# Performance work log

Hardware: AMD Instinct MI355X
Metric: run time of the kernel (lower is better)

Reference implementation:

```python
import jax, jax.numpy as jnp
import numpy as np

N_NODES = 65536
N_PER = 1024      # nodes per graph
NUM_GRAPHS = 64
N_EDGES = 1048576
IN_DIM = 192
PE_DIM = 64
HIDDEN = 256
LATENT = 128
POOL_RATIO = 0.5
K_PER = int(np.ceil(POOL_RATIO * N_PER))  # 512 kept per graph


def setup_inputs() -> dict:
    key = jax.random.key(0)
    ks = jax.random.split(key, 12)
    x_raw = jax.random.normal(ks[0], (N_NODES, IN_DIM), dtype=jnp.float32)
    sincos_pe = jax.random.normal(ks[1], (N_NODES, PE_DIM), dtype=jnp.float32)
    edge_index = jax.random.randint(ks[2], (2, N_EDGES), 0, N_NODES, dtype=jnp.int64)
    batch = (jnp.arange(N_NODES, dtype=jnp.int64) // N_PER)
    eps = jax.random.normal(ks[3], (N_NODES, LATENT), dtype=jnp.float32)
    # learned parameters (GCNConv: Linear no-bias weight + separate bias; TopKPooling weight)
    def glorot(k, shape):
        lim = float(np.sqrt(6.0 / (shape[0] + shape[1])))
        return jax.random.uniform(k, shape, jnp.float32, -lim, lim)
    W1 = glorot(ks[4], (IN_DIM + PE_DIM, HIDDEN))
    b1 = jnp.zeros((HIDDEN,), jnp.float32)
    Wmu = glorot(ks[5], (HIDDEN, LATENT))
    bmu = jnp.zeros((LATENT,), jnp.float32)
    Wlv = glorot(ks[6], (HIDDEN, LATENT))
    blv = jnp.zeros((LATENT,), jnp.float32)
    w_pool = jax.random.uniform(ks[7], (LATENT,), jnp.float32, -1.0, 1.0) / np.sqrt(LATENT)
    return {"x_raw": x_raw, "sincos_pe": sincos_pe, "edge_index": edge_index,
            "batch": batch, "eps": eps, "W1": W1, "b1": b1, "Wmu": Wmu,
            "bmu": bmu, "Wlv": Wlv, "blv": blv, "w_pool": w_pool}


def _gcn_conv(x, W, b, src, dst, n):
    # PyG GCNConv: x' = D^{-1/2}(A+I)D^{-1/2} (x W) + b, self-loops already in src/dst
    h = x @ W                                   # [N, out]
    deg = jnp.zeros((n,), h.dtype).at[dst].add(1.0)
    dinv = jax.lax.rsqrt(deg)                   # deg >= 1 thanks to self-loops
    norm = dinv[src] * dinv[dst]                # [E+N]
    msg = norm[:, None] * h[src]                # gather (irregular)
    return jax.ops.segment_sum(msg, dst, num_segments=n) + b


def reference(x_raw, sincos_pe, edge_index, batch, eps, W1, b1, Wmu, bmu, Wlv, blv, w_pool):
    n = x_raw.shape[0]
    loops = jnp.arange(n, dtype=edge_index.dtype)
    src = jnp.concatenate([edge_index[0], loops])
    dst = jnp.concatenate([edge_index[1], loops])

    x_in = jnp.concatenate([x_raw, sincos_pe], axis=-1)
    h = jax.nn.relu(_gcn_conv(x_in, W1, b1, src, dst, n))
    mu = _gcn_conv(h, Wmu, bmu, src, dst, n)
    logvar = _gcn_conv(h, Wlv, blv, src, dst, n)
    z = mu + eps * jnp.exp(0.5 * logvar)

    # TopKPooling: score = tanh((z . w)/||w||); keep top ratio per graph
    score = jnp.tanh((z @ w_pool) / jnp.linalg.norm(w_pool))   # [N]
    s2 = score.reshape(NUM_GRAPHS, N_PER)
    _, idx = jax.lax.top_k(s2, K_PER)                           # descending per graph
    perm = (idx + (jnp.arange(NUM_GRAPHS) * N_PER)[:, None]).reshape(-1)
    z_pool = z[perm] * score[perm][:, None]
    mu_pool = mu[perm]
    logvar_pool = logvar[perm]
    batch_pool = batch[perm]
    return z_pool, mu_pool, logvar_pool, batch_pool, perm
```

## Files before the change

### kernel.cpp

```cpp
#include <hip/hip_runtime.h>
#include <hip/hip_fp16.h>
#include <math.h>

#define NN      65536
#define NE      1048576
#define NPER    1024
#define NGRAPH  64
#define KPER    512
#define IND     192
#define PED     64
#define HID     256
#define LAT     128

#define OFF_CNT     0u
#define OFF_ROWPTR  65536u
#define OFF_CUR     132096u
#define OFF_DINV    198656u
#define OFF_EPK     264192u
#define OFF_INVWN   2361344u
#define OFF_KEEP    2361360u
#define OFF_SCORE   2395136u
#define OFF_WT1     2460672u
#define OFF_WT2     2493440u
#define OFF_T0B     2526208u
#define OFF_HB      6720512u
#define OFF_MUB     6720512u
#define OFF_LVB     10914816u

#define OUT_MU      4194304
#define OUT_LV      8388608
#define OUT_BATCH   12582912
#define OUT_PERM    12615680

typedef __attribute__((ext_vector_type(8))) short short8;
typedef __attribute__((ext_vector_type(4))) float floatx4;

__device__ __forceinline__ unsigned short f2bf(float f) {
    unsigned int u = __float_as_uint(f);
    u += 0x7FFFu + ((u >> 16) & 1u);
    return (unsigned short)(u >> 16);
}
__device__ __forceinline__ float bf2f(unsigned short u) {
    return __uint_as_float(((unsigned int)u) << 16);
}
__device__ __forceinline__ unsigned int pack2bf(float x, float y) {
    const unsigned int ux = __float_as_uint(x) + 0x8000u;
    const unsigned int uy = __float_as_uint(y) + 0x8000u;
    return __builtin_amdgcn_perm(uy, ux, 0x07060302u);
}
__device__ __forceinline__ unsigned char f2e5(float f) {
    unsigned short u = __half_as_ushort(__float2half(f));
    u += (unsigned short)(0x7Fu + ((u >> 8) & 1u));
    return (unsigned char)(u >> 8);
}
__device__ __forceinline__ void store_bf8x4(unsigned char* base, float v0, float v1, float v2, float v3) {
#if __has_builtin(__builtin_amdgcn_cvt_pk_bf8_f32)
    const unsigned int r01 = (unsigned int)__builtin_amdgcn_cvt_pk_bf8_f32(v0, v1, 0, false);
    const unsigned int r23 = (unsigned int)__builtin_amdgcn_cvt_pk_bf8_f32(v2, v3, 0, false);
    base[0]   = (unsigned char)r01;
    base[256] = (unsigned char)(r01 >> 8);
    base[512] = (unsigned char)r23;
    base[768] = (unsigned char)(r23 >> 8);
#else
    base[0] = f2e5(v0); base[256] = f2e5(v1); base[512] = f2e5(v2); base[768] = f2e5(v3);
#endif
}
__device__ __forceinline__ __half2 e5lo(unsigned int u) {
    return __builtin_bit_cast(__half2, __builtin_amdgcn_perm(u, 0u, 0x05000400u));
}
__device__ __forceinline__ __half2 e5hi(unsigned int u) {
    return __builtin_bit_cast(__half2, __builtin_amdgcn_perm(u, 0u, 0x07000600u));
}

__global__ __launch_bounds__(256) void k_count(const int* __restrict__ ei, int* __restrict__ cnt) {
    int e = blockIdx.x * 256 + threadIdx.x;
    atomicAdd(&cnt[ei[NE + e]], 1);
}

__global__ __launch_bounds__(1024) void k_scan(const int* __restrict__ cnt, int* __restrict__ rp,
                                               float* __restrict__ dinv) {
    __shared__ int part[1024];
    const int t = threadIdx.x;
    const int base = t * 64;
    int loc[64];
#pragma unroll
    for (int i = 0; i < 64; i += 4)
        *(int4*)&loc[i] = *(const int4*)(cnt + base + i);
    int s = 0;
#pragma unroll
    for (int i = 0; i < 64; ++i) s += loc[i];
    part[t] = s;
    __syncthreads();
    for (int d = 1; d < 1024; d <<= 1) {
        int v = (t >= d) ? part[t - d] : 0;
        __syncthreads();
        part[t] += v;
        __syncthreads();
    }
    int run = part[t] - s;
    int rpo[64];
    float dv[64];
#pragma unroll
    for (int i = 0; i < 64; ++i) {
        rpo[i] = run;
        run += loc[i];
        dv[i] = 1.0f / sqrtf((float)(loc[i] + 1));
    }
#pragma unroll
    for (int i = 0; i < 64; i += 4) {
        *(int4*)(rp + base + i) = *(int4*)&rpo[i];
        *(float4*)(dinv + base + i) = *(float4*)&dv[i];
    }
    if (t == 1023) rp[NN] = run;
}

__global__ __launch_bounds__(256) void k_scatter(const int* __restrict__ ei, const int* __restrict__ rp,
                                                 int* __restrict__ cur, const float* __restrict__ dinv,
                                                 int2* __restrict__ epk) {
    int e = blockIdx.x * 256 + threadIdx.x;
    int s = ei[e];
    int d = ei[NE + e];
    int pos = rp[d] + atomicAdd(&cur[d], 1);
    epk[pos] = make_int2(s, __float_as_int(dinv[s] * dinv[d]));
}

__global__ __launch_bounds__(128) void k_wnorm(const float* __restrict__ wp, float* __restrict__ invwn) {
    __shared__ float red[128];
    int t = threadIdx.x;
    float v = wp[t];
    red[t] = v * v;
    __syncthreads();
    for (int s = 64; s > 0; s >>= 1) {
        if (t < s) red[t] += red[t + s];
        __syncthreads();
    }
    if (t == 0) invwn[0] = 1.0f / sqrtf(red[0]);
}

__global__ __launch_bounds__(256) void k_prepw(const float* __restrict__ W1, const float* __restrict__ Wmu,
                                               const float* __restrict__ Wlv, unsigned short* __restrict__ wt1,
                                               unsigned short* __restrict__ wt2) {
    const int n = blockIdx.x, k = threadIdx.x;
    wt1[n * 256 + k] = f2bf(W1[k * 256 + n]);
    wt2[n * 256 + k] = f2bf((n < 128) ? Wmu[k * 128 + n] : Wlv[k * 128 + (n - 128)]);
}

template <int MODE>
__global__ __launch_bounds__(256, 2) void k_gemm(const float* __restrict__ A0f, const float* __restrict__ A1f,
                                                 const unsigned short* __restrict__ Ah,
                                                 const unsigned short* __restrict__ Wt,
                                                 unsigned char* __restrict__ Cb) {
    __shared__ unsigned short lds[2][12288];
    const int tid = threadIdx.x;
    const int w = __builtin_amdgcn_readfirstlane(tid >> 6);
    const int lane = tid & 63;
    const int l = lane & 15, q = lane >> 4;
    const int Rbase = blockIdx.x * 128;
    const int mtb = (w >> 1) * 4;
    const int ntb = (w & 1) * 8;

    const int rs = tid >> 1;
    const int ch = tid & 1;
    const int stile = rs >> 4, sl = rs & 15, q0 = ch * 2;
    const int uA = (stile * 4 + q0) * 16 + sl;

    floatx4 acc[8][4];
#pragma unroll
    for (int j = 0; j < 8; ++j)
#pragma unroll
        for (int m = 0; m < 4; ++m) acc[j][m] = (floatx4)0.0f;

    auto stage = [&](int ks, int buf) {
        if (MODE == 0) {
            const float* p; int ld, col;
            const int k = ks * 32 + ch * 16;
            if (ks < 6) { p = A0f; ld = IND; col = k; }
            else        { p = A1f; ld = PED; col = k - IND; }
            const float* src = p + (size_t)(Rbase + rs) * ld + col;
            unsigned int pk[8];
#pragma unroll
            for (int j = 0; j < 16; j += 4) {
                const float4 t = *(const float4*)(src + j);
                pk[j / 2]     = pack2bf(t.x, t.y);
                pk[j / 2 + 1] = pack2bf(t.z, t.w);
            }
            *(uint4*)&lds[buf][uA * 8]        = *(uint4*)&pk[0];
            *(uint4*)&lds[buf][(uA + 16) * 8] = *(uint4*)&pk[4];
        } else {
            const unsigned short* src = Ah + (size_t)(Rbase + rs) * 256 + ks * 32 + ch * 16;
            *(uint4*)&lds[buf][uA * 8]        = ((const uint4*)src)[0];
            *(uint4*)&lds[buf][(uA + 16) * 8] = ((const uint4*)src)[1];
        }
#pragma unroll
        for (int rep = 0; rep < 2; ++rep) {
            const int n = rep * 128 + rs;
            const unsigned short* srcB = Wt + (size_t)n * 256 + ks * 32 + ch * 16;
            const uint4 w0 = ((const uint4*)srcB)[0];
            const uint4 w1 = ((const uint4*)srcB)[1];
            const int uB = ((n >> 4) * 4 + q0) * 16 + (n & 15);
            *(uint4*)&lds[buf][4096 + uB * 8]        = w0;
            *(uint4*)&lds[buf][4096 + (uB + 16) * 8] = w1;
        }
    };

    stage(0, 0);
    __syncthreads();
#pragma unroll
    for (int ks = 0; ks < 8; ++ks) {
        const int cur = ks & 1;
        if (ks < 7) stage(ks + 1, cur ^ 1);
        short8 a[4];
#pragma unroll
        for (int m = 0; m < 4; ++m)
            a[m] = *(const short8*)&lds[cur][(((mtb + m) * 4 + q) * 16 + l) * 8];
#pragma unroll
        for (int j = 0; j < 8; ++j) {
            const short8 b = *(const short8*)&lds[cur][4096 + (((ntb + j) * 4 + q) * 16 + l) * 8];
#pragma unroll
            for (int m = 0; m < 4; ++m)
                acc[j][m] = __builtin_amdgcn_mfma_f32_16x16x32_bf16(a[m], b, acc[j][m], 0, 0, 0);
        }
        if (ks < 7) __syncthreads();
    }

#pragma unroll
    for (int m = 0; m < 4; ++m) {
        const int mt = mtb + m;
#pragma unroll
        for (int j = 0; j < 8; ++j) {
            const int nt = ntb + j;
            const floatx4 v = acc[j][m];
            unsigned char* base = Cb + (size_t)(Rbase + mt * 16 + q * 4) * 256 + nt * 16 + l;
            store_bf8x4(base, v[0], v[1], v[2], v[3]);
        }
    }
}

__device__ __forceinline__ unsigned int gath(const unsigned char* tbc, int srcv) {
    return *(const unsigned int*)(tbc + ((size_t)__builtin_amdgcn_readfirstlane(srcv) << 8));
}

template <int PHASE>
__global__ __launch_bounds__(256) void k_agg(const unsigned char* __restrict__ tb, const int* __restrict__ rp,
                                             const int2* __restrict__ epk, const float* __restrict__ dinv,
                                             const float* __restrict__ bias0, const float* __restrict__ bias1,
                                             const float* __restrict__ eps, const float* __restrict__ wp,
                                             const float* __restrict__ invwn, unsigned short* __restrict__ hb,
                                             unsigned short* __restrict__ mub, unsigned short* __restrict__ lvb,
                                             float* __restrict__ score) {
    const int wv = __builtin_amdgcn_readfirstlane(threadIdx.x >> 6);
    const int lane = threadIdx.x & 63;
    const int node = blockIdx.x * 4 + wv;
    const int c0 = lane * 4;
    const float di = dinv[node];
    const unsigned char* tbc = tb + c0;

    const unsigned int vs = *(const unsigned int*)(tbc + ((size_t)node << 8));
    const __half2 ws2 = __float2half2_rn(di * di);
    __half2 a01 = __hmul2(ws2, e5lo(vs));
    __half2 a23 = __hmul2(ws2, e5hi(vs));
    __half2 b01 = __float2half2_rn(0.0f);
    __half2 b23 = __float2half2_rn(0.0f);

    const int beg = rp[node], end = rp[node + 1];
    int p = beg;
    if (p + 8 <= end) {
        int2 em[8], en[8];
        unsigned int v[8];
#pragma unroll
        for (int i = 0; i < 8; ++i) em[i] = epk[p + i];
#pragma unroll
        for (int i = 0; i < 8; ++i) v[i] = gath(tbc, em[i].x);
#pragma unroll
        for (int i = 0; i < 8; ++i) en[i] = epk[p + 8 + i];
        while (p + 16 <= end) {
            int2 ef[8];
#pragma unroll
            for (int i = 0; i < 8; ++i) ef[i] = epk[p + 16 + i];
            unsigned int u[8];
#pragma unroll
            for (int i = 0; i < 8; ++i) u[i] = gath(tbc, en[i].x);
#pragma unroll
            for (int i = 0; i < 8; i += 2) {
                const __half2 wA = __float2half2_rn(__int_as_float(em[i].y));
                const __half2 wB = __float2half2_rn(__int_as_float(em[i + 1].y));
                a01 = __hfma2(wA, e5lo(v[i]), a01);     a23 = __hfma2(wA, e5hi(v[i]), a23);
                b01 = __hfma2(wB, e5lo(v[i + 1]), b01); b23 = __hfma2(wB, e5hi(v[i + 1]), b23);
            }
#pragma unroll
            for (int i = 0; i < 8; ++i) { em[i] = en[i]; en[i] = ef[i]; v[i] = u[i]; }
            p += 8;
        }
#pragma unroll
        for (int i = 0; i < 8; i += 2) {
            const __half2 wA = __float2half2_rn(__int_as_float(em[i].y));
            const __half2 wB = __float2half2_rn(__int_as_float(em[i + 1].y));
            a01 = __hfma2(wA, e5lo(v[i]), a01);     a23 = __hfma2(wA, e5hi(v[i]), a23);
            b01 = __hfma2(wB, e5lo(v[i + 1]), b01); b23 = __hfma2(wB, e5hi(v[i + 1]), b23);
        }
        p += 8;
    }
    if (p + 4 <= end) {
        const int2 e0 = epk[p], e1 = epk[p + 1], e2 = epk[p + 2], e3 = epk[p + 3];
        const unsigned int v0 = gath(tbc, e0.x);
        const unsigned int v1 = gath(tbc, e1.x);
        const unsigned int v2 = gath(tbc, e2.x);
        const unsigned int v3 = gath(tbc, e3.x);
        const __half2 w0 = __float2half2_rn(__int_as_float(e0.y));
        const __half2 w1 = __float2half2_rn(__int_as_float(e1.y));
        const __half2 w2 = __float2half2_rn(__int_as_float(e2.y));
        const __half2 w3 = __float2half2_rn(__int_as_float(e3.y));
        a01 = __hfma2(w0, e5lo(v0), a01); a23 = __hfma2(w0, e5hi(v0), a23);
        b01 = __hfma2(w1, e5lo(v1), b01); b23 = __hfma2(w1, e5hi(v1), b23);
        a01 = __hfma2(w2, e5lo(v2), a01); a23 = __hfma2(w2, e5hi(v2), a23);
        b01 = __hfma2(w3, e5lo(v3), b01); b23 = __hfma2(w3, e5hi(v3), b23);
        p += 4;
    }
    for (; p < end; ++p) {
        const int2 e = epk[p];
        const unsigned int v = gath(tbc, e.x);
        const __half2 w2 = __float2half2_rn(__int_as_float(e.y));
        a01 = __hfma2(w2, e5lo(v), a01);
        a23 = __hfma2(w2, e5hi(v), a23);
    }
    a01 = __hadd2(a01, b01);
    a23 = __hadd2(a23, b23);
    const float2 flo = __half22float2(a01);
    const float2 fhi = __half22float2(a23);
    float4 acc = make_float4(flo.x, flo.y, fhi.x, fhi.y);

    if (PHASE == 0) {
        const float4 bb = *(const float4*)(bias0 + c0);
        ushort4 r;
        r.x = f2bf(fmaxf(acc.x + bb.x, 0.0f));
        r.y = f2bf(fmaxf(acc.y + bb.y, 0.0f));
        r.z = f2bf(fmaxf(acc.z + bb.z, 0.0f));
        r.w = f2bf(fmaxf(acc.w + bb.w, 0.0f));
        *(ushort4*)(hb + ((size_t)node << 8) + c0) = r;
    } else {
        const int cb = (lane & 31) * 4;
        const float* bias = (lane < 32) ? bias0 : bias1;
        const float4 bb = *(const float4*)(bias + cb);
        acc.x += bb.x; acc.y += bb.y; acc.z += bb.z; acc.w += bb.w;
        unsigned short* dst = (lane < 32) ? mub : lvb;
        ushort4 st;
        st.x = f2bf(acc.x); st.y = f2bf(acc.y); st.z = f2bf(acc.z); st.w = f2bf(acc.w);
        *(ushort4*)(dst + (size_t)node * 128 + cb) = st;
        float4 l4;
        l4.x = __shfl(acc.x, lane | 32, 64);
        l4.y = __shfl(acc.y, lane | 32, 64);
        l4.z = __shfl(acc.z, lane | 32, 64);
        l4.w = __shfl(acc.w, lane | 32, 64);
        float partial = 0.0f;
        if (lane < 32) {
            const float4 e4 = *(const float4*)(eps + (size_t)node * 128 + cb);
            const float4 w4 = *(const float4*)(wp + cb);
            float zx = fmaf(e4.x, expf(0.5f * l4.x), acc.x);
            float zy = fmaf(e4.y, expf(0.5f * l4.y), acc.y);
            float zz = fmaf(e4.z, expf(0.5f * l4.z), acc.z);
            float zw = fmaf(e4.w, expf(0.5f * l4.w), acc.w);
            partial = zx * w4.x + zy * w4.y + zz * w4.z + zw * w4.w;
        }
        for (int off = 16; off > 0; off >>= 1) partial += __shfl_xor(partial, off, 64);
        if (lane == 0) score[node] = tanhf(partial * invwn[0]);
    }
}

__global__ __launch_bounds__(512) void k_topk(const float* __restrict__ score, const int* __restrict__ batch,
                                              int* __restrict__ keep, float* __restrict__ out) {
    __shared__ float sk[1024];
    __shared__ int si[1024];
    const int g = blockIdx.x, t = threadIdx.x;
    for (int i = t; i < 1024; i += 512) {
        sk[i] = score[g * 1024 + i];
        si[i] = i;
    }
    __syncthreads();
    for (int k = 2; k <= 1024; k <<= 1) {
        for (int j = k >> 1; j > 0; j >>= 1) {
            for (int base = 0; base < 1024; base += 512) {
                int i = base + t;
                int ixj = i ^ j;
                if (ixj > i) {
                    float a = sk[i], b = sk[ixj];
                    int ia = si[i], ib = si[ixj];
                    bool before = (a > b) || (a == b && ia < ib);
                    bool up = ((i & k) == 0);
                    bool sw = up ? (!before) : before;
                    if (sw) {
                        sk[i] = b; si[i] = ib;
                        sk[ixj] = a; si[ixj] = ia;
                    }
                }
            }
            __syncthreads();
        }
    }
    if (t < KPER) {
        int node = g * 1024 + si[t];
        keep[g * KPER + t] = node;
        out[OUT_BATCH + g * KPER + t] = (float)batch[node];
        out[OUT_PERM + g * KPER + t] = (float)node;
    }
}

__global__ __launch_bounds__(128) void k_gather(const int* __restrict__ keep,
                                                const unsigned short* __restrict__ mub,
                                                const unsigned short* __restrict__ lvb,
                                                const float* __restrict__ eps,
                                                const float* __restrict__ score, float* __restrict__ out) {
    const int kidx = blockIdx.x;
    const int c = threadIdx.x;
    const int node = keep[kidx];
    const float m = bf2f(mub[(size_t)node * 128 + c]);
    const float l = bf2f(lvb[(size_t)node * 128 + c]);
    const float e = eps[(size_t)node * 128 + c];
    const float z = fmaf(e, expf(0.5f * l), m);
    const float s = score[node];
    out[(size_t)kidx * 128 + c] = z * s;
    out[OUT_MU + (size_t)kidx * 128 + c] = m;
    out[OUT_LV + (size_t)kidx * 128 + c] = l;
}

extern "C" void kernel_launch(void* const* d_in, const int* in_sizes, int n_in,
                              void* d_out, int out_size, void* d_ws, size_t ws_size,
                              hipStream_t stream) {
    (void)in_sizes; (void)n_in; (void)out_size; (void)ws_size;
    const float* x_raw = (const float*)d_in[0];
    const float* pe    = (const float*)d_in[1];
    const int*   ei    = (const int*)d_in[2];
    const int*   batch = (const int*)d_in[3];
    const float* eps   = (const float*)d_in[4];
    const float* W1    = (const float*)d_in[5];
    const float* b1    = (const float*)d_in[6];
    const float* Wmu   = (const float*)d_in[7];
    const float* bmu   = (const float*)d_in[8];
    const float* Wlv   = (const float*)d_in[9];
    const float* blv   = (const float*)d_in[10];
    const float* wp    = (const float*)d_in[11];
    float* ws = (float*)d_ws;
    int*  iws = (int*)d_ws;
    int2* epk = (int2*)(iws + OFF_EPK);
    unsigned short* wt1  = (unsigned short*)(ws + OFF_WT1);
    unsigned short* wt2  = (unsigned short*)(ws + OFF_WT2);
    unsigned char*  t0b  = (unsigned char*)(ws + OFF_T0B);
    unsigned short* hb16 = (unsigned short*)(ws + OFF_HB);
    unsigned short* mub  = (unsigned short*)(ws + OFF_MUB);
    unsigned short* lvb  = (unsigned short*)(ws + OFF_LVB);
    float* out = (float*)d_out;

    hipMemsetAsync(iws + OFF_CNT, 0, 65536 * 4, stream);
    hipMemsetAsync(iws + OFF_CUR, 0, 65536 * 4, stream);

    k_count<<<NE / 256, 256, 0, stream>>>(ei, iws + OFF_CNT);
    k_scan<<<1, 1024, 0, stream>>>(iws + OFF_CNT, iws + OFF_ROWPTR, ws + OFF_DINV);
    k_scatter<<<NE / 256, 256, 0, stream>>>(ei, iws + OFF_ROWPTR, iws + OFF_CUR, ws + OFF_DINV, epk);
    k_wnorm<<<1, 128, 0, stream>>>(wp, ws + OFF_INVWN);
    k_prepw<<<256, 256, 0, stream>>>(W1, Wmu, Wlv, wt1, wt2);

    k_gemm<0><<<NN / 128, 256, 0, stream>>>(x_raw, pe, nullptr, wt1, t0b);
    k_agg<0><<<NN / 4, 256, 0, stream>>>(t0b, iws + OFF_ROWPTR, epk, ws + OFF_DINV,
                                         b1, nullptr, nullptr, nullptr, nullptr,
                                         hb16, nullptr, nullptr, nullptr);
    k_gemm<1><<<NN / 128, 256, 0, stream>>>(nullptr, nullptr, hb16, wt2, t0b);
    k_agg<1><<<NN / 4, 256, 0, stream>>>(t0b, iws + OFF_ROWPTR, epk, ws + OFF_DINV,
                                         bmu, blv, eps, wp, ws + OFF_INVWN,
                                         nullptr, mub, lvb, ws + OFF_SCORE);
    k_topk<<<NGRAPH, 512, 0, stream>>>(ws + OFF_SCORE, batch, iws + OFF_KEEP, out);
    k_gather<<<NGRAPH * KPER, 128, 0, stream>>>(iws + OFF_KEEP, mub, lvb, eps,
                                                ws + OFF_SCORE, out);
}
```

Baseline: 439.9 us.

## Parallelize CSR scan, vectorize count, pack GEMM bf8 stores, lane-load edges in agg

Result: faster. 422.3 us (-4.0%).

```diff
diff --git a/kernel.cpp b/kernel.cpp
--- a/kernel.cpp
+++ b/kernel.cpp
@@ -53,16 +53,13 @@
     u += (unsigned short)(0x7Fu + ((u >> 8) & 1u));
     return (unsigned char)(u >> 8);
 }
-__device__ __forceinline__ void store_bf8x4(unsigned char* base, float v0, float v1, float v2, float v3) {
+__device__ __forceinline__ unsigned int pack4e5(float v0, float v1, float v2, float v3) {
 #if __has_builtin(__builtin_amdgcn_cvt_pk_bf8_f32)
-    const unsigned int r01 = (unsigned int)__builtin_amdgcn_cvt_pk_bf8_f32(v0, v1, 0, false);
-    const unsigned int r23 = (unsigned int)__builtin_amdgcn_cvt_pk_bf8_f32(v2, v3, 0, false);
-    base[0]   = (unsigned char)r01;
-    base[256] = (unsigned char)(r01 >> 8);
-    base[512] = (unsigned char)r23;
-    base[768] = (unsigned char)(r23 >> 8);
+    const int t0 = __builtin_amdgcn_cvt_pk_bf8_f32(v0, v1, 0, false);
+    return (unsigned int)__builtin_amdgcn_cvt_pk_bf8_f32(v2, v3, t0, true);
 #else
-    base[0] = f2e5(v0); base[256] = f2e5(v1); base[512] = f2e5(v2); base[768] = f2e5(v3);
+    return (unsigned int)f2e5(v0) | ((unsigned int)f2e5(v1) << 8) |
+           ((unsigned int)f2e5(v2) << 16) | ((unsigned int)f2e5(v3) << 24);
 #endif
 }
 __device__ __forceinline__ __half2 e5lo(unsigned int u) {
@@ -73,45 +70,53 @@
 }
 
 __global__ __launch_bounds__(256) void k_count(const int* __restrict__ ei, int* __restrict__ cnt) {
-    int e = blockIdx.x * 256 + threadIdx.x;
-    atomicAdd(&cnt[ei[NE + e]], 1);
-}
-
-__global__ __launch_bounds__(1024) void k_scan(const int* __restrict__ cnt, int* __restrict__ rp,
-                                               float* __restrict__ dinv) {
-    __shared__ int part[1024];
+    const int g = blockIdx.x * 256 + threadIdx.x;
+    const int4 d4 = *(const int4*)(ei + NE + g * 4);
+    atomicAdd(&cnt[d4.x], 1);
+    atomicAdd(&cnt[d4.y], 1);
+    atomicAdd(&cnt[d4.z], 1);
+    atomicAdd(&cnt[d4.w], 1);
+}
+
+__global__ __launch_bounds__(256) void k_scanA(const int* __restrict__ cnt, int* __restrict__ rp,
+                                               float* __restrict__ dinv, int* __restrict__ bsum) {
+    __shared__ int sh[256];
+    const int t = threadIdx.x, b = blockIdx.x;
+    const int i = b * 256 + t;
+    const int c = cnt[i];
+    sh[t] = c;
+    __syncthreads();
+    for (int d = 1; d < 256; d <<= 1) {
+        const int v = (t >= d) ? sh[t - d] : 0;
+        __syncthreads();
+        sh[t] += v;
+        __syncthreads();
+    }
+    rp[i] = sh[t] - c;
+    dinv[i] = 1.0f / sqrtf((float)(c + 1));
+    if (t == 255) bsum[b] = sh[t];
+}
+
+__global__ __launch_bounds__(256) void k_scanB(int* __restrict__ bsum) {
+    __shared__ int sh[256];
     const int t = threadIdx.x;
-    const int base = t * 64;
-    int loc[64];
-#pragma unroll
-    for (int i = 0; i < 64; i += 4)
-        *(int4*)&loc[i] = *(const int4*)(cnt + base + i);
-    int s = 0;
-#pragma unroll
-    for (int i = 0; i < 64; ++i) s += loc[i];
-    part[t] = s;
+    const int c = bsum[t];
+    sh[t] = c;
     __syncthreads();
-    for (int d = 1; d < 1024; d <<= 1) {
-        int v = (t >= d) ? part[t - d] : 0;
+    for (int d = 1; d < 256; d <<= 1) {
+        const int v = (t >= d) ? sh[t - d] : 0;
         __syncthreads();
-        part[t] += v;
+        sh[t] += v;
         __syncthreads();
     }
-    int run = part[t] - s;
-    int rpo[64];
-    float dv[64];
-#pragma unroll
-    for (int i = 0; i < 64; ++i) {
-        rpo[i] = run;
-        run += loc[i];
-        dv[i] = 1.0f / sqrtf((float)(loc[i] + 1));
-    }
-#pragma unroll
-    for (int i = 0; i < 64; i += 4) {
-        *(int4*)(rp + base + i) = *(int4*)&rpo[i];
-        *(float4*)(dinv + base + i) = *(float4*)&dv[i];
-    }
-    if (t == 1023) rp[NN] = run;
+    bsum[t] = sh[t] - c;
+}
+
+__global__ __launch_bounds__(256) void k_scanC(int* __restrict__ rp, const int* __restrict__ bsum) {
+    const int t = threadIdx.x, b = blockIdx.x;
+    const int i = b * 256 + t;
+    rp[i] += bsum[b];
+    if (i == NN - 1) rp[NN] = NE;
 }
 
 __global__ __launch_bounds__(256) void k_scatter(const int* __restrict__ ei, const int* __restrict__ rp,
@@ -218,26 +223,20 @@
             const short8 b = *(const short8*)&lds[cur][4096 + (((ntb + j) * 4 + q) * 16 + l) * 8];
 #pragma unroll
             for (int m = 0; m < 4; ++m)
-                acc[j][m] = __builtin_amdgcn_mfma_f32_16x16x32_bf16(a[m], b, acc[j][m], 0, 0, 0);
+                acc[j][m] = __builtin_amdgcn_mfma_f32_16x16x32_bf16(b, a[m], acc[j][m], 0, 0, 0);
         }
         if (ks < 7) __syncthreads();
     }
 
 #pragma unroll
     for (int m = 0; m < 4; ++m) {
-        const int mt = mtb + m;
+        unsigned char* rbase = Cb + (size_t)(Rbase + (mtb + m) * 16 + l) * 256 + q * 4;
 #pragma unroll
         for (int j = 0; j < 8; ++j) {
-            const int nt = ntb + j;
             const floatx4 v = acc[j][m];
-            unsigned char* base = Cb + (size_t)(Rbase + mt * 16 + q * 4) * 256 + nt * 16 + l;
-            store_bf8x4(base, v[0], v[1], v[2], v[3]);
-        }
-    }
-}
-
-__device__ __forceinline__ unsigned int gath(const unsigned char* tbc, int srcv) {
-    return *(const unsigned int*)(tbc + ((size_t)__builtin_amdgcn_readfirstlane(srcv) << 8));
+            *(unsigned int*)(rbase + (ntb + j) * 16) = pack4e5(v[0], v[1], v[2], v[3]);
+        }
+    }
 }
 
 template <int PHASE>
@@ -262,39 +261,38 @@
     __half2 b01 = __float2half2_rn(0.0f);
     __half2 b23 = __float2half2_rn(0.0f);
 
+    const int lane8 = lane & 7;
     const int beg = rp[node], end = rp[node + 1];
     int p = beg;
     if (p + 8 <= end) {
-        int2 em[8], en[8];
+        int2 emv = epk[p + lane8];
+        int2 env = epk[p + 8 + lane8];
         unsigned int v[8];
 #pragma unroll
-        for (int i = 0; i < 8; ++i) em[i] = epk[p + i];
-#pragma unroll
-        for (int i = 0; i < 8; ++i) v[i] = gath(tbc, em[i].x);
-#pragma unroll
-        for (int i = 0; i < 8; ++i) en[i] = epk[p + 8 + i];
+        for (int i = 0; i < 8; ++i)
+            v[i] = *(const unsigned int*)(tbc + ((size_t)__builtin_amdgcn_readlane(emv.x, i) << 8));
         while (p + 16 <= end) {
-            int2 ef[8];
-#pragma unroll
-            for (int i = 0; i < 8; ++i) ef[i] = epk[p + 16 + i];
+            const int2 efv = epk[p + 16 + lane8];
             unsigned int u[8];
 #pragma unroll
-            for (int i = 0; i < 8; ++i) u[i] = gath(tbc, en[i].x);
+            for (int i = 0; i < 8; ++i)
+                u[i] = *(const unsigned int*)(tbc + ((size_t)__builtin_amdgcn_readlane(env.x, i) << 8));
 #pragma unroll
             for (int i = 0; i < 8; i += 2) {
-                const __half2 wA = __float2half2_rn(__int_as_float(em[i].y));
-                const __half2 wB = __float2half2_rn(__int_as_float(em[i + 1].y));
+                const __half2 wA = __float2half2_rn(__int_as_float(__builtin_amdgcn_readlane(emv.y, i)));
+                const __half2 wB = __float2half2_rn(__int_as_float(__builtin_amdgcn_readlane(emv.y, i + 1)));
                 a01 = __hfma2(wA, e5lo(v[i]), a01);     a23 = __hfma2(wA, e5hi(v[i]), a23);
                 b01 = __hfma2(wB, e5lo(v[i + 1]), b01); b23 = __hfma2(wB, e5hi(v[i + 1]), b23);
             }
-#pragma unroll
-            for (int i = 0; i < 8; ++i) { em[i] = en[i]; en[i] = ef[i]; v[i] = u[i]; }
+            emv = env; env = efv;
+#pragma unroll
+            for (int i = 0; i < 8; ++i) v[i] = u[i];
             p += 8;
         }
 #pragma unroll
         for (int i = 0; i < 8; i += 2) {
-            const __half2 wA = __float2half2_rn(__int_as_float(em[i].y));
-            const __half2 wB = __float2half2_rn(__int_as_float(em[i + 1].y));
+            const __half2 wA = __float2half2_rn(__int_as_float(__builtin_amdgcn_readlane(emv.y, i)));
+            const __half2 wB = __float2half2_rn(__int_as_float(__builtin_amdgcn_readlane(emv.y, i + 1)));
             a01 = __hfma2(wA, e5lo(v[i]), a01);     a23 = __hfma2(wA, e5hi(v[i]), a23);
             b01 = __hfma2(wB, e5lo(v[i + 1]), b01); b23 = __hfma2(wB, e5hi(v[i + 1]), b23);
         }
@@ -302,10 +300,10 @@
     }
     if (p + 4 <= end) {
         const int2 e0 = epk[p], e1 = epk[p + 1], e2 = epk[p + 2], e3 = epk[p + 3];
-        const unsigned int v0 = gath(tbc, e0.x);
-        const unsigned int v1 = gath(tbc, e1.x);
-        const unsigned int v2 = gath(tbc, e2.x);
-        const unsigned int v3 = gath(tbc, e3.x);
+        const unsigned int v0 = *(const unsigned int*)(tbc + ((size_t)__builtin_amdgcn_readfirstlane(e0.x) << 8));
+        const unsigned int v1 = *(const unsigned int*)(tbc + ((size_t)__builtin_amdgcn_readfirstlane(e1.x) << 8));
+        const unsigned int v2 = *(const unsigned int*)(tbc + ((size_t)__builtin_amdgcn_readfirstlane(e2.x) << 8));
+        const unsigned int v3 = *(const unsigned int*)(tbc + ((size_t)__builtin_amdgcn_readfirstlane(e3.x) << 8));
         const __half2 w0 = __float2half2_rn(__int_as_float(e0.y));
         const __half2 w1 = __float2half2_rn(__int_as_float(e1.y));
         const __half2 w2 = __float2half2_rn(__int_as_float(e2.y));
@@ -318,7 +316,7 @@
     }
     for (; p < end; ++p) {
         const int2 e = epk[p];
-        const unsigned int v = gath(tbc, e.x);
+        const unsigned int v = *(const unsigned int*)(tbc + ((size_t)__builtin_amdgcn_readfirstlane(e.x) << 8));
         const __half2 w2 = __float2half2_rn(__int_as_float(e.y));
         a01 = __hfma2(w2, e5lo(v), a01);
         a23 = __hfma2(w2, e5hi(v), a23);
@@ -452,8 +450,10 @@
     hipMemsetAsync(iws + OFF_CNT, 0, 65536 * 4, stream);
     hipMemsetAsync(iws + OFF_CUR, 0, 65536 * 4, stream);
 
-    k_count<<<NE / 256, 256, 0, stream>>>(ei, iws + OFF_CNT);
-    k_scan<<<1, 1024, 0, stream>>>(iws + OFF_CNT, iws + OFF_ROWPTR, ws + OFF_DINV);
+    k_count<<<NE / 1024, 256, 0, stream>>>(ei, iws + OFF_CNT);
+    k_scanA<<<256, 256, 0, stream>>>(iws + OFF_CNT, iws + OFF_ROWPTR, ws + OFF_DINV, iws + OFF_KEEP);
+    k_scanB<<<1, 256, 0, stream>>>(iws + OFF_KEEP);
+    k_scanC<<<256, 256, 0, stream>>>(iws + OFF_ROWPTR, iws + OFF_KEEP);
     k_scatter<<<NE / 256, 256, 0, stream>>>(ei, iws + OFF_ROWPTR, iws + OFF_CUR, ws + OFF_DINV, epk);
     k_wnorm<<<1, 128, 0, stream>>>(wp, ws + OFF_INVWN);
     k_prepw<<<256, 256, 0, stream>>>(W1, Wmu, Wlv, wt1, wt2);
```
